# Optimization experiments

Measured on AMD Instinct MI355X. Metric: run time of the kernel, lower is better.

Reference implementation:

```python
import jax, jax.numpy as jnp
import numpy as np

B = 4
NS = [65536, 16384, 4096, 1024, 256]   # nodes per mesh level
DEG = 16                               # avg degree
KORD = 6                               # Chebyshev polynomial order
FE = [3, 16, 16, 16, 32]               # encoder filters
FD = [32, 16, 16, 16, 16, 3]           # decoder filters
Z = 64                                 # latent dim


def cheb_norm(edge_index, n):
    # symmetric normalization D^-1/2 A D^-1/2 per ChebConv_Coma.norm
    row, col = edge_index
    deg = jnp.zeros((n,), jnp.float32).at[row].add(jnp.ones(row.shape, jnp.float32))
    dis = jnp.where(deg > 0, deg ** -0.5, 0.0)
    return dis[row] * dis[col]


def propagate(x, row, col, norm):
    # out[b, row] += norm * x[b, col]   (sparse adjacency matvec, batched)
    return jnp.zeros_like(x).at[:, row].add(x[:, col] * norm[None, :, None])


def cheb_conv(x, edge_index, norm, W, b):
    # Chebyshev recursion: T0 = x, T1 = L x, Tk = 2 L T_{k-1} - T_{k-2}
    row, col = edge_index
    Tx0 = x
    out = jnp.einsum('bnf,fg->bng', Tx0, W[0])
    Tx1 = propagate(x, row, col, norm)
    out = out + jnp.einsum('bnf,fg->bng', Tx1, W[1])
    for k in range(2, W.shape[0]):
        Tx2 = 2.0 * propagate(Tx1, row, col, norm) - Tx0
        out = out + jnp.einsum('bnf,fg->bng', Tx2, W[k])
        Tx0, Tx1 = Tx1, Tx2
    return out + b if b is not None else out


def pool(x, idx, w):
    # sparse pooling matmul: 3 nnz per output row; idx/w: [Nout, 3]
    return jnp.einsum('bnkf,nk->bnf', x[:, idx], w)


def coma_forward(x, eis, dids, dws, uids, uws, encW, encB, decW, decB,
                 enc_w, enc_b, dec_w, dec_b):
    norms = [cheb_norm(eis[i], NS[i]) for i in range(5)]
    h = x.reshape(B, NS[0], FE[0])
    # encoder: cheb conv + relu + downsample pool, 4 levels
    for i in range(4):
        h = jax.nn.relu(cheb_conv(h, eis[i], norms[i], encW[i], encB[i]))
        h = pool(h, dids[i], dws[i])
    h = h.reshape(B, NS[-1] * FE[-1])
    z = jax.nn.relu(h @ enc_w + enc_b)
    # decoder
    h = jax.nn.relu(z @ dec_w + dec_b).reshape(B, NS[-1], FD[0])
    for i in range(4):
        lvl = 3 - i
        h = pool(h, uids[lvl], uws[lvl])
        h = jax.nn.relu(cheb_conv(h, eis[lvl], norms[lvl], decW[i], decB[i]))
    h = cheb_conv(h, eis[0], norms[0], decW[4], None)  # last conv, no bias
    return h.reshape(-1, FE[0])


def setup_inputs() -> dict:
    key = jax.random.key(0)
    ks = iter(jax.random.split(key, 80))
    inp = {}
    inp['x'] = jax.random.normal(next(ks), (B * NS[0], FE[0]), jnp.float32)
    for i, n in enumerate(NS):
        inp[f'ei{i}'] = jax.random.randint(next(ks), (2, DEG * n), 0, n)
    for i in range(4):
        inp[f'down_i{i}'] = jax.random.randint(next(ks), (NS[i + 1], 3), 0, NS[i])
        inp[f'down_w{i}'] = jax.random.uniform(next(ks), (NS[i + 1], 3), jnp.float32)
        inp[f'up_i{i}'] = jax.random.randint(next(ks), (NS[i], 3), 0, NS[i + 1])
        inp[f'up_w{i}'] = jax.random.uniform(next(ks), (NS[i], 3), jnp.float32)
    for i in range(4):
        inp[f'ew{i}'] = 0.1 * jax.random.normal(next(ks), (KORD, FE[i], FE[i + 1]), jnp.float32)
        inp[f'eb{i}'] = jnp.zeros((FE[i + 1],), jnp.float32)
    for i in range(5):
        inp[f'dw{i}'] = 0.1 * jax.random.normal(next(ks), (KORD, FD[i], FD[i + 1]), jnp.float32)
    for i in range(4):
        inp[f'db{i}'] = jnp.zeros((FD[i + 1],), jnp.float32)
    inp['enc_w'] = 0.1 * jax.random.normal(next(ks), (NS[-1] * FE[-1], Z), jnp.float32)
    inp['enc_b'] = 0.1 * jnp.ones((Z,), jnp.float32)
    inp['dec_w'] = 0.1 * jax.random.normal(next(ks), (Z, FD[0] * NS[-1]), jnp.float32)
    inp['dec_b'] = 0.1 * jnp.ones((FD[0] * NS[-1],), jnp.float32)
    return inp


def reference(x, ei0, ei1, ei2, ei3, ei4,
              down_i0, down_w0, up_i0, up_w0,
              down_i1, down_w1, up_i1, up_w1,
              down_i2, down_w2, up_i2, up_w2,
              down_i3, down_w3, up_i3, up_w3,
              ew0, eb0, ew1, eb1, ew2, eb2, ew3, eb3,
              dw0, dw1, dw2, dw3, dw4, db0, db1, db2, db3,
              enc_w, enc_b, dec_w, dec_b):
    eis = [ei0, ei1, ei2, ei3, ei4]
    dids = [down_i0, down_i1, down_i2, down_i3]
    dws = [down_w0, down_w1, down_w2, down_w3]
    uids = [up_i0, up_i1, up_i2, up_i3]
    uws = [up_w0, up_w1, up_w2, up_w3]
    encW = [ew0, ew1, ew2, ew3]
    encB = [eb0, eb1, eb2, eb3]
    decW = [dw0, dw1, dw2, dw3, dw4]
    decB = [db0, db1, db2, db3]
    return coma_forward(x, eis, dids, dws, uids, uws, encW, encB, decW, decB,
                        enc_w, enc_b, dec_w, dec_b)
```

## Files before the change

kernel.cpp:

```cpp
#include <hip/hip_runtime.h>

#define TPB 256

static constexpr int B_ = 4;
static constexpr int DEG_ = 16;

using u16 = unsigned short;

static constexpr int LB0 = 0, LB1 = 65536, LB2 = 81920, LB3 = 86016, LB4 = 87040;
static constexpr int CE0 = 0, CE1 = 1048576, CE2 = 1310720, CE3 = 1376256, CE4 = 1392640;


__device__ inline float b2f(u16 u) { return __uint_as_float((unsigned)u << 16); }
__device__ inline u16 f2b(float f) {
    unsigned b = __float_as_uint(f);
    b += 0x7fffu + ((b >> 16) & 1u);
    return (u16)(b >> 16);
}

template<int F>
__device__ inline void load_row_bf16(const u16* __restrict__ p, float* v) {
    if constexpr (F % 8 == 0) {
        #pragma unroll
        for (int i = 0; i < F / 8; ++i) {
            uint4 raw = reinterpret_cast<const uint4*>(p)[i];
            unsigned rr[4] = {raw.x, raw.y, raw.z, raw.w};
            #pragma unroll
            for (int k = 0; k < 4; ++k) {
                v[i * 8 + 2 * k]     = __uint_as_float(rr[k] << 16);
                v[i * 8 + 2 * k + 1] = __uint_as_float(rr[k] & 0xffff0000u);
            }
        }
    } else {
        #pragma unroll
        for (int f = 0; f < F; ++f) v[f] = b2f(p[f]);
    }
}

template<int F>
__device__ inline void store_row_bf16(u16* __restrict__ p, const float* v) {
    if constexpr (F % 8 == 0) {
        #pragma unroll
        for (int i = 0; i < F / 8; ++i) {
            uint4 raw;
            unsigned* rr = &raw.x;
            #pragma unroll
            for (int k = 0; k < 4; ++k)
                rr[k] = (unsigned)f2b(v[i * 8 + 2 * k]) |
                        ((unsigned)f2b(v[i * 8 + 2 * k + 1]) << 16);
            reinterpret_cast<uint4*>(p)[i] = raw;
        }
    } else {
        #pragma unroll
        for (int f = 0; f < F; ++f) p[f] = f2b(v[f]);
    }
}


__global__ void cnt_kernel(const int* __restrict__ row, int* __restrict__ cnt, int E) {
    int e = blockIdx.x * blockDim.x + threadIdx.x;
    if (e < E) atomicAdd(&cnt[row[e]], 1);
}

__global__ void scanA_kernel(const int* __restrict__ cnt, int* __restrict__ partial,
                             int* __restrict__ bsum) {
    __shared__ int sdata[256];
    int tid = threadIdx.x;
    int base = blockIdx.x * 1024 + tid * 4;
    int v0 = cnt[base], v1 = cnt[base + 1], v2 = cnt[base + 2], v3 = cnt[base + 3];
    int tsum = v0 + v1 + v2 + v3;
    sdata[tid] = tsum;
    __syncthreads();
    for (int ofs = 1; ofs < 256; ofs <<= 1) {
        int x = (tid >= ofs) ? sdata[tid - ofs] : 0;
        __syncthreads();
        sdata[tid] += x;
        __syncthreads();
    }
    int excl = sdata[tid] - tsum;
    partial[base] = excl;         excl += v0;
    partial[base + 1] = excl;     excl += v1;
    partial[base + 2] = excl;     excl += v2;
    partial[base + 3] = excl;
    if (tid == 255) bsum[blockIdx.x] = sdata[255];
}

__global__ void scanB_kernel(int* __restrict__ bsum, int nb) {
    __shared__ int s[128];
    int tid = threadIdx.x;
    int v = tid < nb ? bsum[tid] : 0;
    s[tid] = v;
    __syncthreads();
    for (int ofs = 1; ofs < 128; ofs <<= 1) {
        int x = (tid >= ofs) ? s[tid - ofs] : 0;
        __syncthreads();
        s[tid] += x;
        __syncthreads();
    }
    if (tid < nb) bsum[tid] = s[tid] - v;
}

__global__ void scanC_kernel(const int* __restrict__ partial, const int* __restrict__ bsum,
                             int* __restrict__ rp0, int* __restrict__ rp1,
                             int* __restrict__ rp2, int* __restrict__ rp3) {
    int i = blockIdx.x * blockDim.x + threadIdx.x;
    if (i >= LB4) return;
    int g = partial[i] + bsum[i >> 10];
    if (i < LB1)      rp0[i - LB0] = g - CE0;
    else if (i < LB2) rp1[i - LB1] = g - CE1;
    else if (i < LB3) rp2[i - LB2] = g - CE2;
    else              rp3[i - LB3] = g - CE3;
    if (i == 0) {
        rp0[LB1 - LB0] = CE1 - CE0;
        rp1[LB2 - LB1] = CE2 - CE1;
        rp2[LB3 - LB2] = CE3 - CE2;
        rp3[LB4 - LB3] = CE4 - CE3;
    }
}

__global__ void fill_kernel(const int* __restrict__ row, const int* __restrict__ col,
                            const int* __restrict__ rowptr, int* __restrict__ cur,
                            const int* __restrict__ cnt, int* __restrict__ ccol,
                            float* __restrict__ cw, int E) {
    int e = blockIdx.x * blockDim.x + threadIdx.x;
    if (e >= E) return;
    int r = row[e], c = col[e];
    int pos = rowptr[r] + atomicAdd(&cur[r], 1);
    float dr = cnt[r] > 0 ? rsqrtf((float)cnt[r]) : 0.f;
    float dc = cnt[c] > 0 ? rsqrtf((float)cnt[c]) : 0.f;
    ccol[pos] = c;
    cw[pos] = dr * dc;
}


__global__ void f2b_tr_kernel(const float* __restrict__ in, u16* __restrict__ out, int N) {
    int t = blockIdx.x * blockDim.x + threadIdx.x;
    if (t >= B_ * N * 3) return;
    int f = t % 3;
    int nb = t / 3;
    int b = nb & 3;
    int n = nb >> 2;
    out[t] = f2b(in[((size_t)b * N + n) * 3 + f]);
}

template<int F, int G, bool FIRST, bool LAST, bool OSTD>
__global__ __launch_bounds__(256) void cheb_sweep(
    const u16* __restrict__ gsrc, const u16* __restrict__ selfp, u16* __restrict__ dst,
    const int* __restrict__ rowptr, const int* __restrict__ ccol,
    const float* __restrict__ cw, const float* __restrict__ Wk,
    const float* __restrict__ bias, float* __restrict__ out,
    u16* __restrict__ mirror, int N, int relu)
{
    constexpr int WSZ = (FIRST ? 2 : 1) * F * G;
    __shared__ float sW[WSZ];
    for (int i = threadIdx.x; i < WSZ; i += 256) sW[i] = Wk[i];
    __syncthreads();
    int t = blockIdx.x * 256 + (int)threadIdx.x;
    if (t >= B_ * N) return;
    int r = t >> 2;
    int b = t & 3;
    const float alpha = FIRST ? 1.0f : 2.0f;

    float sv[F];
    load_row_bf16<F>(selfp + (size_t)t * F, sv);
    float tv[F];
    #pragma unroll
    for (int f = 0; f < F; ++f) tv[f] = FIRST ? 0.f : -sv[f];

    int beg = rowptr[r], end = rowptr[r + 1];
    for (int j = beg; j < end; ++j) {
        int c = ccol[j];
        float w = alpha * cw[j];
        float gv[F];
        load_row_bf16<F>(gsrc + (size_t)((c << 2) | b) * F, gv);
        #pragma unroll
        for (int f = 0; f < F; ++f) tv[f] += w * gv[f];
    }
    if (!LAST) store_row_bf16<F>(dst + (size_t)t * F, tv);

    float acc[G];
    float* orow = OSTD ? out + ((size_t)b * N + r) * G : out + (size_t)t * G;
    if (FIRST) {
        #pragma unroll
        for (int g = 0; g < G; ++g) acc[g] = 0.f;
        #pragma unroll
        for (int f = 0; f < F; ++f) {
            float xv = sv[f];
            #pragma unroll
            for (int g = 0; g < G; ++g) acc[g] += xv * sW[f * G + g];
        }
        #pragma unroll
        for (int f = 0; f < F; ++f) {
            float tvf = tv[f];
            #pragma unroll
            for (int g = 0; g < G; ++g) acc[g] += tvf * sW[F * G + f * G + g];
        }
    } else {
        #pragma unroll
        for (int g = 0; g < G; ++g) acc[g] = orow[g];
        #pragma unroll
        for (int f = 0; f < F; ++f) {
            float tvf = tv[f];
            #pragma unroll
            for (int g = 0; g < G; ++g) acc[g] += tvf * sW[f * G + g];
        }
    }
    if (LAST) {
        if (bias) {
            #pragma unroll
            for (int g = 0; g < G; ++g) acc[g] += bias[g];
        }
        if (relu) {
            #pragma unroll
            for (int g = 0; g < G; ++g) acc[g] = fmaxf(acc[g], 0.f);
        }
        if (mirror) {
            store_row_bf16<G>(mirror + (size_t)t * G, acc);
            return;
        }
    }
    #pragma unroll
    for (int g = 0; g < G; ++g) orow[g] = acc[g];
}


__global__ void pool_kernel(const float* __restrict__ in, u16* __restrict__ out,
                            const int* __restrict__ idx, const float* __restrict__ w,
                            int Nin, int Nout, int F) {
    int t = blockIdx.x * blockDim.x + threadIdx.x;
    if (t >= B_ * Nout * F) return;
    int f = t % F;
    int nb = t / F;
    int b = nb & 3;
    int n = nb >> 2;
    float acc = 0.f;
    for (int k = 0; k < 3; ++k) {
        int src = idx[n * 3 + k];
        acc += w[n * 3 + k] * in[(size_t)((src << 2) | b) * F + f];
    }
    out[t] = f2b(acc);
}

__global__ void dense_enc_kernel(const u16* __restrict__ h, const float* __restrict__ W,
                                 const float* __restrict__ bias, float* __restrict__ z) {
    int b = blockIdx.x >> 6;
    int g = blockIdx.x & 63;
    int tid = threadIdx.x;
    float acc = 0.f;
    for (int i = tid; i < 8192; i += 256) {
        int n = i >> 5, f = i & 31;
        acc += b2f(h[(((size_t)n << 2) | b) * 32 + f]) * W[(size_t)i * 64 + g];
    }
    __shared__ float red[256];
    red[tid] = acc;
    __syncthreads();
    for (int sft = 128; sft > 0; sft >>= 1) {
        if (tid < sft) red[tid] += red[tid + sft];
        __syncthreads();
    }
    if (tid == 0) z[b * 64 + g] = fmaxf(red[0] + bias[g], 0.f);
}

__global__ void dense_dec_kernel(const float* __restrict__ z, const float* __restrict__ W,
                                 const float* __restrict__ bias, float* __restrict__ out) {
    int t = blockIdx.x * blockDim.x + threadIdx.x;
    if (t >= B_ * 8192) return;
    int b = t / 8192, j = t % 8192;
    float acc = bias[j];
    for (int k = 0; k < 64; ++k) acc += z[b * 64 + k] * W[(size_t)k * 8192 + j];
    int n = j >> 5, f = j & 31;
    out[(((size_t)n << 2) | b) * 32 + f] = fmaxf(acc, 0.f);
}


static inline unsigned cdivu(size_t a, size_t b) { return (unsigned)((a + b - 1) / b); }

template<int F, int G, bool OSTD = false>
static void run_cheb(const u16* X, u16* TP, u16* TQ, float* out,
                     const float* Wk, const float* bias, int relu, u16* mirror,
                     const int* rp, const int* cc, const float* cwp, int N, hipStream_t s) {
    const size_t FG = (size_t)F * G;
    unsigned g = cdivu((size_t)B_ * N, 256);
    cheb_sweep<F, G, true, false, OSTD><<<g, 256, 0, s>>>(X, X, TP, rp, cc, cwp,
                                                    Wk, nullptr, out, nullptr, N, 0);
    cheb_sweep<F, G, false, false, OSTD><<<g, 256, 0, s>>>(TP, X, TQ, rp, cc, cwp,
                                                     Wk + 2 * FG, nullptr, out, nullptr, N, 0);
    cheb_sweep<F, G, false, false, OSTD><<<g, 256, 0, s>>>(TQ, TP, TP, rp, cc, cwp,
                                                     Wk + 3 * FG, nullptr, out, nullptr, N, 0);
    cheb_sweep<F, G, false, false, OSTD><<<g, 256, 0, s>>>(TP, TQ, TQ, rp, cc, cwp,
                                                     Wk + 4 * FG, nullptr, out, nullptr, N, 0);
    cheb_sweep<F, G, false, true, OSTD><<<g, 256, 0, s>>>(TQ, TP, nullptr, rp, cc, cwp,
                                                    Wk + 5 * FG, bias, out, mirror, N, relu);
}

extern "C" void kernel_launch(void* const* d_in, const int* in_sizes, int n_in,
                              void* d_out, int out_size, void* d_ws, size_t ws_size,
                              hipStream_t stream) {
    (void)in_sizes; (void)n_in; (void)out_size; (void)ws_size;
    hipStream_t s = stream;

    static const int NS_[5] = {65536, 16384, 4096, 1024, 256};
    static const int LBa[5] = {LB0, LB1, LB2, LB3, LB4};

    const float* x = (const float*)d_in[0];
    const int* ei[4];
    for (int l = 0; l < 4; ++l) ei[l] = (const int*)d_in[1 + l];
    const int* down_i[4]; const float* down_w[4];
    const int* up_i[4];   const float* up_w[4];
    for (int i = 0; i < 4; ++i) {
        down_i[i] = (const int*)d_in[6 + 4 * i];
        down_w[i] = (const float*)d_in[7 + 4 * i];
        up_i[i]   = (const int*)d_in[8 + 4 * i];
        up_w[i]   = (const float*)d_in[9 + 4 * i];
    }
    const float* encW[4]; const float* encB[4];
    for (int i = 0; i < 4; ++i) {
        encW[i] = (const float*)d_in[22 + 2 * i];
        encB[i] = (const float*)d_in[23 + 2 * i];
    }
    const float* decW[5];
    for (int i = 0; i < 5; ++i) decW[i] = (const float*)d_in[30 + i];
    const float* decB[4];
    for (int i = 0; i < 4; ++i) decB[i] = (const float*)d_in[35 + i];
    const float* enc_w = (const float*)d_in[39];
    const float* enc_b = (const float*)d_in[40];
    const float* dec_w = (const float*)d_in[41];
    const float* dec_b = (const float*)d_in[42];

    float* ws = (float*)d_ws;
    size_t off = 0;
    const size_t SLOT = (size_t)B_ * 65536 * 16;
    float* BA = ws + off; off += SLOT;
    u16* XB = (u16*)(ws + off); off += SLOT / 2;
    u16* TP = (u16*)(ws + off); off += SLOT / 2;
    u16* TQ = (u16*)(ws + off); off += SLOT / 2;
    int* cntAll = (int*)(ws + off); off += LB4;
    int* curAll = (int*)(ws + off); off += LB4;
    int* partial = (int*)(ws + off); off += LB4;
    int* bsum = (int*)(ws + off); off += 128;
    int* rowptr[4]; int* ccol[4]; float* cwz[4];
    for (int l = 0; l < 4; ++l) {
        int N = NS_[l], E = DEG_ * N;
        rowptr[l] = (int*)(ws + off); off += (size_t)N + 4;
        ccol[l]   = (int*)(ws + off); off += (size_t)E;
        cwz[l]    = ws + off;         off += (size_t)E;
    }
    float* zbuf = ws + off; off += 256;

    hipMemsetAsync(cntAll, 0, (size_t)LB4 * sizeof(int), s);
    hipMemsetAsync(curAll, 0, (size_t)LB4 * sizeof(int), s);
    for (int l = 0; l < 4; ++l) {
        int E = DEG_ * NS_[l];
        cnt_kernel<<<cdivu(E, TPB), TPB, 0, s>>>(ei[l], cntAll + LBa[l], E);
    }
    scanA_kernel<<<85, 256, 0, s>>>(cntAll, partial, bsum);
    scanB_kernel<<<1, 128, 0, s>>>(bsum, 85);
    scanC_kernel<<<cdivu(LB4, TPB), TPB, 0, s>>>(partial, bsum,
                                                 rowptr[0], rowptr[1], rowptr[2], rowptr[3]);
    for (int l = 0; l < 4; ++l) {
        int E = DEG_ * NS_[l];
        fill_kernel<<<cdivu(E, TPB), TPB, 0, s>>>(ei[l], ei[l] + E, rowptr[l],
                                                  curAll + LBa[l], cntAll + LBa[l],
                                                  ccol[l], cwz[l], E);
    }

    f2b_tr_kernel<<<cdivu((size_t)B_ * 65536 * 3, TPB), TPB, 0, s>>>(x, XB, 65536);
    run_cheb<3, 16>(XB, TP, TQ, BA, encW[0], encB[0], 1, nullptr,
                    rowptr[0], ccol[0], cwz[0], NS_[0], s);
    pool_kernel<<<cdivu((size_t)B_ * NS_[1] * 16, TPB), TPB, 0, s>>>(
        BA, XB, down_i[0], down_w[0], NS_[0], NS_[1], 16);
    run_cheb<16, 16>(XB, TP, TQ, BA, encW[1], encB[1], 1, nullptr,
                     rowptr[1], ccol[1], cwz[1], NS_[1], s);
    pool_kernel<<<cdivu((size_t)B_ * NS_[2] * 16, TPB), TPB, 0, s>>>(
        BA, XB, down_i[1], down_w[1], NS_[1], NS_[2], 16);
    run_cheb<16, 16>(XB, TP, TQ, BA, encW[2], encB[2], 1, nullptr,
                     rowptr[2], ccol[2], cwz[2], NS_[2], s);
    pool_kernel<<<cdivu((size_t)B_ * NS_[3] * 16, TPB), TPB, 0, s>>>(
        BA, XB, down_i[2], down_w[2], NS_[2], NS_[3], 16);
    run_cheb<16, 32>(XB, TP, TQ, BA, encW[3], encB[3], 1, nullptr,
                     rowptr[3], ccol[3], cwz[3], NS_[3], s);
    pool_kernel<<<cdivu((size_t)B_ * NS_[4] * 32, TPB), TPB, 0, s>>>(
        BA, XB, down_i[3], down_w[3], NS_[3], NS_[4], 32);

    dense_enc_kernel<<<B_ * 64, 256, 0, s>>>(XB, enc_w, enc_b, zbuf);
    dense_dec_kernel<<<cdivu((size_t)B_ * 8192, TPB), TPB, 0, s>>>(zbuf, dec_w, dec_b, BA);

    pool_kernel<<<cdivu((size_t)B_ * NS_[3] * 32, TPB), TPB, 0, s>>>(
        BA, XB, up_i[3], up_w[3], NS_[4], NS_[3], 32);
    run_cheb<32, 16>(XB, TP, TQ, BA, decW[0], decB[0], 1, nullptr,
                     rowptr[3], ccol[3], cwz[3], NS_[3], s);
    pool_kernel<<<cdivu((size_t)B_ * NS_[2] * 16, TPB), TPB, 0, s>>>(
        BA, XB, up_i[2], up_w[2], NS_[3], NS_[2], 16);
    run_cheb<16, 16>(XB, TP, TQ, BA, decW[1], decB[1], 1, nullptr,
                     rowptr[2], ccol[2], cwz[2], NS_[2], s);
    pool_kernel<<<cdivu((size_t)B_ * NS_[1] * 16, TPB), TPB, 0, s>>>(
        BA, XB, up_i[1], up_w[1], NS_[2], NS_[1], 16);
    run_cheb<16, 16>(XB, TP, TQ, BA, decW[2], decB[2], 1, nullptr,
                     rowptr[1], ccol[1], cwz[1], NS_[1], s);
    pool_kernel<<<cdivu((size_t)B_ * NS_[0] * 16, TPB), TPB, 0, s>>>(
        BA, XB, up_i[0], up_w[0], NS_[1], NS_[0], 16);
    run_cheb<16, 16>(XB, TP, TQ, BA, decW[3], decB[3], 1, XB,
                     rowptr[0], ccol[0], cwz[0], NS_[0], s);
    run_cheb<16, 3, true>(XB, TP, TQ, (float*)d_out, decW[4], nullptr, 0, nullptr,
                          rowptr[0], ccol[0], cwz[0], NS_[0], s);
}
```

Before: 1.208 ms.

## Split Chebyshev sweeps from weight combine, compress edge data, keep activations bf16

Separates the sparse propagation sweeps from the dense weight multiply: five sweep kernels write each Chebyshev term to its own bf16 buffer, and one combine kernel applies all six weight matrices, the bias and the relu. This drops the per-sweep read-modify-write of the fp32 output accumulator. Edge weights are no longer stored; they are rebuilt on the fly from a per-node inverse-sqrt-degree array, and column indices shrink to 16-bit. Intermediate activations between levels are stored as bf16, and blocks drop to 128 threads. The cost is extra buffers, an extra gather of dis[c] per edge, and a grid size computed without rounding up.

```diff
diff --git a/kernel.cpp b/kernel.cpp
--- a/kernel.cpp
+++ b/kernel.cpp
@@ -60,6 +60,11 @@
 __global__ void cnt_kernel(const int* __restrict__ row, int* __restrict__ cnt, int E) {
     int e = blockIdx.x * blockDim.x + threadIdx.x;
     if (e < E) atomicAdd(&cnt[row[e]], 1);
+}
+
+__global__ void dis_kernel(const int* __restrict__ cnt, float* __restrict__ dis, int n) {
+    int i = blockIdx.x * blockDim.x + threadIdx.x;
+    if (i < n) dis[i] = cnt[i] > 0 ? rsqrtf((float)cnt[i]) : 0.f;
 }
 
 __global__ void scanA_kernel(const int* __restrict__ cnt, int* __restrict__ partial,
@@ -120,16 +125,12 @@
 
 __global__ void fill_kernel(const int* __restrict__ row, const int* __restrict__ col,
                             const int* __restrict__ rowptr, int* __restrict__ cur,
-                            const int* __restrict__ cnt, int* __restrict__ ccol,
-                            float* __restrict__ cw, int E) {
+                            u16* __restrict__ ccol, int E) {
     int e = blockIdx.x * blockDim.x + threadIdx.x;
     if (e >= E) return;
-    int r = row[e], c = col[e];
+    int r = row[e];
     int pos = rowptr[r] + atomicAdd(&cur[r], 1);
-    float dr = cnt[r] > 0 ? rsqrtf((float)cnt[r]) : 0.f;
-    float dc = cnt[c] > 0 ? rsqrtf((float)cnt[c]) : 0.f;
-    ccol[pos] = c;
-    cw[pos] = dr * dc;
+    ccol[pos] = (u16)col[e];
 }
 
 
@@ -143,90 +144,92 @@
     out[t] = f2b(in[((size_t)b * N + n) * 3 + f]);
 }
 
-template<int F, int G, bool FIRST, bool LAST, bool OSTD>
-__global__ __launch_bounds__(256) void cheb_sweep(
+template<int F, bool FIRST>
+__global__ __launch_bounds__(128) void sweep_k(
     const u16* __restrict__ gsrc, const u16* __restrict__ selfp, u16* __restrict__ dst,
-    const int* __restrict__ rowptr, const int* __restrict__ ccol,
-    const float* __restrict__ cw, const float* __restrict__ Wk,
-    const float* __restrict__ bias, float* __restrict__ out,
-    u16* __restrict__ mirror, int N, int relu)
+    const int* __restrict__ rowptr, const u16* __restrict__ ccol,
+    const float* __restrict__ dis, int N)
 {
-    constexpr int WSZ = (FIRST ? 2 : 1) * F * G;
-    __shared__ float sW[WSZ];
-    for (int i = threadIdx.x; i < WSZ; i += 256) sW[i] = Wk[i];
-    __syncthreads();
-    int t = blockIdx.x * 256 + (int)threadIdx.x;
+    int t = blockIdx.x * 128 + (int)threadIdx.x;
     if (t >= B_ * N) return;
     int r = t >> 2;
     int b = t & 3;
-    const float alpha = FIRST ? 1.0f : 2.0f;
-
-    float sv[F];
-    load_row_bf16<F>(selfp + (size_t)t * F, sv);
+
     float tv[F];
-    #pragma unroll
-    for (int f = 0; f < F; ++f) tv[f] = FIRST ? 0.f : -sv[f];
-
+    if constexpr (FIRST) {
+        #pragma unroll
+        for (int f = 0; f < F; ++f) tv[f] = 0.f;
+    } else {
+        float sv[F];
+        load_row_bf16<F>(selfp + (size_t)t * F, sv);
+        #pragma unroll
+        for (int f = 0; f < F; ++f) tv[f] = -sv[f];
+    }
+    const float scale = (FIRST ? 1.0f : 2.0f) * dis[r];
     int beg = rowptr[r], end = rowptr[r + 1];
     for (int j = beg; j < end; ++j) {
-        int c = ccol[j];
-        float w = alpha * cw[j];
+        int c = (int)ccol[j];
+        float w = scale * dis[c];
         float gv[F];
         load_row_bf16<F>(gsrc + (size_t)((c << 2) | b) * F, gv);
         #pragma unroll
         for (int f = 0; f < F; ++f) tv[f] += w * gv[f];
     }
-    if (!LAST) store_row_bf16<F>(dst + (size_t)t * F, tv);
+    store_row_bf16<F>(dst + (size_t)t * F, tv);
+}
+
+template<int F, int G, bool OSTD>
+__global__ __launch_bounds__(128) void combine_k(
+    const u16* __restrict__ T0, const u16* __restrict__ T1, const u16* __restrict__ T2,
+    const u16* __restrict__ T3, const u16* __restrict__ T4, const u16* __restrict__ T5,
+    const float* __restrict__ W6, const float* __restrict__ bias,
+    u16* __restrict__ outb, float* __restrict__ outf, int N, int relu)
+{
+    __shared__ float sW[6 * F * G];
+    for (int i = threadIdx.x; i < 6 * F * G; i += 128) sW[i] = W6[i];
+    __syncthreads();
+    int t = blockIdx.x * 128 + (int)threadIdx.x;
+    if (t >= B_ * N) return;
 
     float acc[G];
-    float* orow = OSTD ? out + ((size_t)b * N + r) * G : out + (size_t)t * G;
-    if (FIRST) {
-        #pragma unroll
-        for (int g = 0; g < G; ++g) acc[g] = 0.f;
+    #pragma unroll
+    for (int g = 0; g < G; ++g) acc[g] = 0.f;
+
+    const u16* Ts[6] = {T0, T1, T2, T3, T4, T5};
+    #pragma unroll
+    for (int k = 0; k < 6; ++k) {
+        float tv[F];
+        load_row_bf16<F>(Ts[k] + (size_t)t * F, tv);
+        const float* w = sW + k * F * G;
         #pragma unroll
         for (int f = 0; f < F; ++f) {
-            float xv = sv[f];
+            float x = tv[f];
             #pragma unroll
-            for (int g = 0; g < G; ++g) acc[g] += xv * sW[f * G + g];
+            for (int g = 0; g < G; ++g) acc[g] += x * w[f * G + g];
         }
-        #pragma unroll
-        for (int f = 0; f < F; ++f) {
-            float tvf = tv[f];
-            #pragma unroll
-            for (int g = 0; g < G; ++g) acc[g] += tvf * sW[F * G + f * G + g];
-        }
+    }
+    if (bias) {
+        #pragma unroll
+        for (int g = 0; g < G; ++g) acc[g] += bias[g];
+    }
+    if (relu) {
+        #pragma unroll
+        for (int g = 0; g < G; ++g) acc[g] = fmaxf(acc[g], 0.f);
+    }
+    if (OSTD) {
+        int r = t >> 2, b = t & 3;
+        float* orow = outf + ((size_t)b * N + r) * G;
+        #pragma unroll
+        for (int g = 0; g < G; ++g) orow[g] = acc[g];
     } else {
-        #pragma unroll
-        for (int g = 0; g < G; ++g) acc[g] = orow[g];
-        #pragma unroll
-        for (int f = 0; f < F; ++f) {
-            float tvf = tv[f];
-            #pragma unroll
-            for (int g = 0; g < G; ++g) acc[g] += tvf * sW[f * G + g];
-        }
-    }
-    if (LAST) {
-        if (bias) {
-            #pragma unroll
-            for (int g = 0; g < G; ++g) acc[g] += bias[g];
-        }
-        if (relu) {
-            #pragma unroll
-            for (int g = 0; g < G; ++g) acc[g] = fmaxf(acc[g], 0.f);
-        }
-        if (mirror) {
-            store_row_bf16<G>(mirror + (size_t)t * G, acc);
-            return;
-        }
-    }
-    #pragma unroll
-    for (int g = 0; g < G; ++g) orow[g] = acc[g];
-}
-
-
-__global__ void pool_kernel(const float* __restrict__ in, u16* __restrict__ out,
+        store_row_bf16<G>(outb + (size_t)t * G, acc);
+    }
+}
+
+
+__global__ void pool_kernel(const u16* __restrict__ in, u16* __restrict__ out,
                             const int* __restrict__ idx, const float* __restrict__ w,
-                            int Nin, int Nout, int F) {
+                            int Nout, int F) {
     int t = blockIdx.x * blockDim.x + threadIdx.x;
     if (t >= B_ * Nout * F) return;
     int f = t % F;
@@ -236,7 +239,7 @@
     float acc = 0.f;
     for (int k = 0; k < 3; ++k) {
         int src = idx[n * 3 + k];
-        acc += w[n * 3 + k] * in[(size_t)((src << 2) | b) * F + f];
+        acc += w[n * 3 + k] * b2f(in[(size_t)((src << 2) | b) * F + f]);
     }
     out[t] = f2b(acc);
 }
@@ -262,35 +265,31 @@
 }
 
 __global__ void dense_dec_kernel(const float* __restrict__ z, const float* __restrict__ W,
-                                 const float* __restrict__ bias, float* __restrict__ out) {
+                                 const float* __restrict__ bias, u16* __restrict__ out) {
     int t = blockIdx.x * blockDim.x + threadIdx.x;
     if (t >= B_ * 8192) return;
     int b = t / 8192, j = t % 8192;
     float acc = bias[j];
     for (int k = 0; k < 64; ++k) acc += z[b * 64 + k] * W[(size_t)k * 8192 + j];
     int n = j >> 5, f = j & 31;
-    out[(((size_t)n << 2) | b) * 32 + f] = fmaxf(acc, 0.f);
+    out[(((size_t)n << 2) | b) * 32 + f] = f2b(fmaxf(acc, 0.f));
 }
 
 
 static inline unsigned cdivu(size_t a, size_t b) { return (unsigned)((a + b - 1) / b); }
 
 template<int F, int G, bool OSTD = false>
-static void run_cheb(const u16* X, u16* TP, u16* TQ, float* out,
-                     const float* Wk, const float* bias, int relu, u16* mirror,
-                     const int* rp, const int* cc, const float* cwp, int N, hipStream_t s) {
-    const size_t FG = (size_t)F * G;
-    unsigned g = cdivu((size_t)B_ * N, 256);
-    cheb_sweep<F, G, true, false, OSTD><<<g, 256, 0, s>>>(X, X, TP, rp, cc, cwp,
-                                                    Wk, nullptr, out, nullptr, N, 0);
-    cheb_sweep<F, G, false, false, OSTD><<<g, 256, 0, s>>>(TP, X, TQ, rp, cc, cwp,
-                                                     Wk + 2 * FG, nullptr, out, nullptr, N, 0);
-    cheb_sweep<F, G, false, false, OSTD><<<g, 256, 0, s>>>(TQ, TP, TP, rp, cc, cwp,
-                                                     Wk + 3 * FG, nullptr, out, nullptr, N, 0);
-    cheb_sweep<F, G, false, false, OSTD><<<g, 256, 0, s>>>(TP, TQ, TQ, rp, cc, cwp,
-                                                     Wk + 4 * FG, nullptr, out, nullptr, N, 0);
-    cheb_sweep<F, G, false, true, OSTD><<<g, 256, 0, s>>>(TQ, TP, nullptr, rp, cc, cwp,
-                                                    Wk + 5 * FG, bias, out, mirror, N, relu);
+static void run_cheb(const u16* X, u16* const* T, const float* Wk, const float* bias,
+                     int relu, u16* outb, float* outf,
+                     const int* rp, const u16* cc, const float* dis, int N, hipStream_t s) {
+    unsigned g = (unsigned)((size_t)B_ * N / 128);
+    sweep_k<F, true><<<g, 128, 0, s>>>(X, nullptr, T[0], rp, cc, dis, N);
+    sweep_k<F, false><<<g, 128, 0, s>>>(T[0], X, T[1], rp, cc, dis, N);
+    sweep_k<F, false><<<g, 128, 0, s>>>(T[1], T[0], T[2], rp, cc, dis, N);
+    sweep_k<F, false><<<g, 128, 0, s>>>(T[2], T[1], T[3], rp, cc, dis, N);
+    sweep_k<F, false><<<g, 128, 0, s>>>(T[3], T[2], T[4], rp, cc, dis, N);
+    combine_k<F, G, OSTD><<<g, 128, 0, s>>>(X, T[0], T[1], T[2], T[3], T[4],
+                                            Wk, bias, outb, outf, N, relu);
 }
 
 extern "C" void kernel_launch(void* const* d_in, const int* in_sizes, int n_in,
@@ -301,6 +300,7 @@
 
     static const int NS_[5] = {65536, 16384, 4096, 1024, 256};
     static const int LBa[5] = {LB0, LB1, LB2, LB3, LB4};
+    static const int CEa[5] = {CE0, CE1, CE2, CE3, CE4};
 
     const float* x = (const float*)d_in[0];
     const int* ei[4];
@@ -329,22 +329,19 @@
 
     float* ws = (float*)d_ws;
     size_t off = 0;
-    const size_t SLOT = (size_t)B_ * 65536 * 16;
-    float* BA = ws + off; off += SLOT;
-    u16* XB = (u16*)(ws + off); off += SLOT / 2;
-    u16* TP = (u16*)(ws + off); off += SLOT / 2;
-    u16* TQ = (u16*)(ws + off); off += SLOT / 2;
+    const size_t HSLOT = (size_t)B_ * 65536 * 16 / 2;
+    u16* XA = (u16*)(ws + off); off += HSLOT;
+    u16* XBuf = (u16*)(ws + off); off += HSLOT;
+    u16* T[5];
+    for (int i = 0; i < 5; ++i) { T[i] = (u16*)(ws + off); off += HSLOT; }
     int* cntAll = (int*)(ws + off); off += LB4;
     int* curAll = (int*)(ws + off); off += LB4;
     int* partial = (int*)(ws + off); off += LB4;
     int* bsum = (int*)(ws + off); off += 128;
-    int* rowptr[4]; int* ccol[4]; float* cwz[4];
-    for (int l = 0; l < 4; ++l) {
-        int N = NS_[l], E = DEG_ * N;
-        rowptr[l] = (int*)(ws + off); off += (size_t)N + 4;
-        ccol[l]   = (int*)(ws + off); off += (size_t)E;
-        cwz[l]    = ws + off;         off += (size_t)E;
-    }
+    float* disAll = ws + off; off += LB4;
+    int* rowptr[4];
+    for (int l = 0; l < 4; ++l) { rowptr[l] = (int*)(ws + off); off += (size_t)NS_[l] + 4; }
+    u16* ccolAll = (u16*)(ws + off); off += (CE4 + 1) / 2;
     float* zbuf = ws + off; off += 256;
 
     hipMemsetAsync(cntAll, 0, (size_t)LB4 * sizeof(int), s);
@@ -353,6 +350,7 @@
         int E = DEG_ * NS_[l];
         cnt_kernel<<<cdivu(E, TPB), TPB, 0, s>>>(ei[l], cntAll + LBa[l], E);
     }
+    dis_kernel<<<cdivu(LB4, TPB), TPB, 0, s>>>(cntAll, disAll, LB4);
     scanA_kernel<<<85, 256, 0, s>>>(cntAll, partial, bsum);
     scanB_kernel<<<1, 128, 0, s>>>(bsum, 85);
     scanC_kernel<<<cdivu(LB4, TPB), TPB, 0, s>>>(partial, bsum,
@@ -360,47 +358,49 @@
     for (int l = 0; l < 4; ++l) {
         int E = DEG_ * NS_[l];
         fill_kernel<<<cdivu(E, TPB), TPB, 0, s>>>(ei[l], ei[l] + E, rowptr[l],
-                                                  curAll + LBa[l], cntAll + LBa[l],
-                                                  ccol[l], cwz[l], E);
-    }
-
-    f2b_tr_kernel<<<cdivu((size_t)B_ * 65536 * 3, TPB), TPB, 0, s>>>(x, XB, 65536);
-    run_cheb<3, 16>(XB, TP, TQ, BA, encW[0], encB[0], 1, nullptr,
-                    rowptr[0], ccol[0], cwz[0], NS_[0], s);
+                                                  curAll + LBa[l], ccolAll + CEa[l], E);
+    }
+
+    const float* dis[4]; const u16* cc[4];
+    for (int l = 0; l < 4; ++l) { dis[l] = disAll + LBa[l]; cc[l] = ccolAll + CEa[l]; }
+
+    f2b_tr_kernel<<<cdivu((size_t)B_ * 65536 * 3, TPB), TPB, 0, s>>>(x, XA, 65536);
+    run_cheb<3, 16>(XA, T, encW[0], encB[0], 1, XBuf, nullptr,
+                    rowptr[0], cc[0], dis[0], NS_[0], s);
     pool_kernel<<<cdivu((size_t)B_ * NS_[1] * 16, TPB), TPB, 0, s>>>(
-        BA, XB, down_i[0], down_w[0], NS_[0], NS_[1], 16);
-    run_cheb<16, 16>(XB, TP, TQ, BA, encW[1], encB[1], 1, nullptr,
-                     rowptr[1], ccol[1], cwz[1], NS_[1], s);
+        XBuf, XA, down_i[0], down_w[0], NS_[1], 16);
+    run_cheb<16, 16>(XA, T, encW[1], encB[1], 1, XBuf, nullptr,
+                     rowptr[1], cc[1], dis[1], NS_[1], s);
     pool_kernel<<<cdivu((size_t)B_ * NS_[2] * 16, TPB), TPB, 0, s>>>(
-        BA, XB, down_i[1], down_w[1], NS_[1], NS_[2], 16);
-    run_cheb<16, 16>(XB, TP, TQ, BA, encW[2], encB[2], 1, nullptr,
-                     rowptr[2], ccol[2], cwz[2], NS_[2], s);
+        XBuf, XA, down_i[1], down_w[1], NS_[2], 16);
+    run_cheb<16, 16>(XA, T, encW[2], encB[2], 1, XBuf, nullptr,
+                     rowptr[2], cc[2], dis[2], NS_[2], s);
     pool_kernel<<<cdivu((size_t)B_ * NS_[3] * 16, TPB), TPB, 0, s>>>(
-        BA, XB, down_i[2], down_w[2], NS_[2], NS_[3], 16);
-    run_cheb<16, 32>(XB, TP, TQ, BA, encW[3], encB[3], 1, nullptr,
-                     rowptr[3], ccol[3], cwz[3], NS_[3], s);
+        XBuf, XA, down_i[2], down_w[2], NS_[3], 16);
+    run_cheb<16, 32>(XA, T, encW[3], encB[3], 1, XBuf, nullptr,
+                     rowptr[3], cc[3], dis[3], NS_[3], s);
     pool_kernel<<<cdivu((size_t)B_ * NS_[4] * 32, TPB), TPB, 0, s>>>(
-        BA, XB, down_i[3], down_w[3], NS_[3], NS_[4], 32);
-
-    dense_enc_kernel<<<B_ * 64, 256, 0, s>>>(XB, enc_w, enc_b, zbuf);
-    dense_dec_kernel<<<cdivu((size_t)B_ * 8192, TPB), TPB, 0, s>>>(zbuf, dec_w, dec_b, BA);
+        XBuf, XA, down_i[3], down_w[3], NS_[4], 32);
+
+    dense_enc_kernel<<<B_ * 64, 256, 0, s>>>(XA, enc_w, enc_b, zbuf);
+    dense_dec_kernel<<<cdivu((size_t)B_ * 8192, TPB), TPB, 0, s>>>(zbuf, dec_w, dec_b, XBuf);
 
     pool_kernel<<<cdivu((size_t)B_ * NS_[3] * 32, TPB), TPB, 0, s>>>(
-        BA, XB, up_i[3], up_w[3], NS_[4], NS_[3], 32);
-    run_cheb<32, 16>(XB, TP, TQ, BA, decW[0], decB[0], 1, nullptr,
-                     rowptr[3], ccol[3], cwz[3], NS_[3], s);
+        XBuf, XA, up_i[3], up_w[3], NS_[3], 32);
+    run_cheb<32, 16>(XA, T, decW[0], decB[0], 1, XBuf, nullptr,
+                     rowptr[3], cc[3], dis[3], NS_[3], s);
     pool_kernel<<<cdivu((size_t)B_ * NS_[2] * 16, TPB), TPB, 0, s>>>(
-        BA, XB, up_i[2], up_w[2], NS_[3], NS_[2], 16);
-    run_cheb<16, 16>(XB, TP, TQ, BA, decW[1], decB[1], 1, nullptr,
-                     rowptr[2], ccol[2], cwz[2], NS_[2], s);
+        XBuf, XA, up_i[2], up_w[2], NS_[2], 16);
+    run_cheb<16, 16>(XA, T, decW[1], decB[1], 1, XBuf, nullptr,
+                     rowptr[2], cc[2], dis[2], NS_[2], s);
     pool_kernel<<<cdivu((size_t)B_ * NS_[1] * 16, TPB), TPB, 0, s>>>(
-        BA, XB, up_i[1], up_w[1], NS_[2], NS_[1], 16);
-    run_cheb<16, 16>(XB, TP, TQ, BA, decW[2], decB[2], 1, nullptr,
-                     rowptr[1], ccol[1], cwz[1], NS_[1], s);
+        XBuf, XA, up_i[1], up_w[1], NS_[1], 16);
+    run_cheb<16, 16>(XA, T, decW[2], decB[2], 1, XBuf, nullptr,
+                     rowptr[1], cc[1], dis[1], NS_[1], s);
     pool_kernel<<<cdivu((size_t)B_ * NS_[0] * 16, TPB), TPB, 0, s>>>(
-        BA, XB, up_i[0], up_w[0], NS_[1], NS_[0], 16);
-    run_cheb<16, 16>(XB, TP, TQ, BA, decW[3], decB[3], 1, XB,
-                     rowptr[0], ccol[0], cwz[0], NS_[0], s);
-    run_cheb<16, 3, true>(XB, TP, TQ, (float*)d_out, decW[4], nullptr, 0, nullptr,
-                          rowptr[0], ccol[0], cwz[0], NS_[0], s);
-}
+        XBuf, XA, up_i[0], up_w[0], NS_[0], 16);
+    run_cheb<16, 16>(XA, T, decW[3], decB[3], 1, XBuf, nullptr,
+                     rowptr[0], cc[0], dis[0], NS_[0], s);
+    run_cheb<16, 3, true>(XBuf, T, decW[4], nullptr, 0, nullptr, (float*)d_out,
+                          rowptr[0], cc[0], dis[0], NS_[0], s);
+}
```

After: 1.136 ms. 6.0% less time.
